# Kernel optimization log

Hardware: AMD Instinct MI355X
Metric: run time of the kernel (lower is better)

Reference implementation:

```python
import jax, jax.numpy as jnp
import numpy as np

S, B, D, H, DH = 2048, 2, 512, 8, 64
SCALE = 1.0 / DH ** 0.5
EPS = 1e-5
LN_EPS = 1e-5


def setup_inputs() -> dict:
    key = jax.random.key(0)
    k1, k2, k3, k4 = jax.random.split(key, 4)
    h = jax.random.normal(k1, (S, B, D), dtype=jnp.float32)
    # causal mask, True = masked out, shape [qlen, klen, 1] (dim==3 branch)
    attn_mask = jnp.triu(jnp.ones((S, S), dtype=bool), k=1)[:, :, None]
    Wq = jax.random.normal(k2, (D, H * DH), dtype=jnp.float32) * 0.02
    Wkv = jax.random.normal(k3, (D, 2 * H * DH), dtype=jnp.float32) * 0.02
    Wo = jax.random.normal(k4, (H * DH, D), dtype=jnp.float32) * 0.02
    gamma = jnp.ones((D,), dtype=jnp.float32)
    beta = jnp.zeros((D,), dtype=jnp.float32)
    return {"h": h, "Wq": Wq, "Wkv": Wkv, "Wo": Wo,
            "gamma": gamma, "beta": beta, "attn_mask": attn_mask}


def _layer_norm(x, gamma, beta):
    mu = jnp.mean(x, axis=-1, keepdims=True)
    var = jnp.mean(jnp.square(x - mu), axis=-1, keepdims=True)
    return (x - mu) * jax.lax.rsqrt(var + LN_EPS) * gamma + beta


def reference(h, Wq, Wkv, Wo, gamma, beta, attn_mask):
    # mems=None, pre_lnorm=False, dropout=dropatt=0 (eval)
    c = h
    head_q = (h @ Wq).reshape(S, B, H, DH)
    kv = (c @ Wkv)
    head_k, head_v = jnp.split(kv, 2, axis=-1)
    head_k = head_k.reshape(S, B, H, DH)
    head_v = head_v.reshape(S, B, H, DH)
    # elu(x) + 1 feature map
    head_q = jax.nn.elu(head_q) + 1.0
    head_k = jax.nn.elu(head_k) + 1.0
    # quadratic score matrix [i, j, b, n]
    attn_score = jnp.einsum('ibnd,jbnd->ijbn', head_q, head_k) * SCALE
    # dim==3 mask: [qlen, klen, 1] -> [qlen, klen, 1, 1], fill with 0
    attn_score = jnp.where(attn_mask[:, :, :, None], 0.0, attn_score)
    # sum-normalize over key axis (dim 1 = j)
    denominator = jnp.sum(attn_score, axis=1, keepdims=True) + EPS
    attn_prob = attn_score / denominator
    attn_vec = jnp.einsum('ijbn,jbnd->ibnd', attn_prob, head_v)
    attn_vec = attn_vec.reshape(S, B, H * DH)
    attn_out = attn_vec @ Wo
    # post-lnorm residual
    return _layer_norm(h + attn_out, gamma, beta)
```

## Files before the change

### kernel.cpp

```cpp
#include <hip/hip_runtime.h>
#include <hip/hip_bf16.h>
#include <math.h>

#define SCALE 0.125f
#define EPS 1e-5f
#define LN_EPS 1e-5f

typedef short short8 __attribute__((ext_vector_type(8)));
typedef float floatx4 __attribute__((ext_vector_type(4)));
typedef unsigned short us;

__device__ __forceinline__ float elu1(float x) { return x > 0.f ? x + 1.f : __expf(x); }
__device__ __forceinline__ us f2bf(float f) {
    __hip_bfloat16 b = __float2bfloat16(f);
    return __builtin_bit_cast(us, b);
}
__device__ __forceinline__ void gload_lds16(const void* g, void* lds) {
    __builtin_amdgcn_global_load_lds(
        (const __attribute__((address_space(1))) unsigned int*)g,
        (__attribute__((address_space(3))) unsigned int*)lds, 16, 0, 0);
}
__device__ __forceinline__ floatx4 mfma_bf16(short8 a, short8 b, floatx4 c) {
    return __builtin_amdgcn_mfma_f32_16x16x32_bf16(a, b, c, 0, 0, 0);
}

__global__ __launch_bounds__(256)
void pack_kernel(const float* __restrict__ h, const float* __restrict__ Wq,
                 const float* __restrict__ Wkv, const float* __restrict__ Wo,
                 us* __restrict__ hB, us* __restrict__ WqkvT, us* __restrict__ WoT,
                 us* __restrict__ VTg) {
    const int bid = blockIdx.x, tid = threadIdx.x;
    if (bid < 2048) {
        int idx = bid * 1024 + tid * 4;
        float4 v = *(const float4*)(h + idx);
        ushort4 o;
        o.x = f2bf(v.x); o.y = f2bf(v.y); o.z = f2bf(v.z); o.w = f2bf(v.w);
        *(ushort4*)(hB + idx) = o;
        return;
    }
    if (bid < 2304) {
        __shared__ us T[64][72];
        const float* src; int ld, n0s, k0; us* dst;
        if (bid < 2240) {
            int t2 = bid - 2048;
            int nt = t2 % 24, kt = t2 / 24;
            int n0 = nt * 64; k0 = kt * 64;
            if (n0 < 512) { src = Wq; ld = 512; n0s = n0; }
            else          { src = Wkv; ld = 1024; n0s = n0 - 512; }
            dst = WqkvT + (size_t)n0 * 512;
        } else {
            int t2 = bid - 2240;
            int nt = t2 & 7, kt = t2 >> 3;
            src = Wo; ld = 512; n0s = nt * 64; k0 = kt * 64;
            dst = WoT + (size_t)(nt * 64) * 512;
        }
        {
            int k = tid >> 2, cs = (tid & 3) * 16;
            const float* p = src + (size_t)(k0 + k) * ld + n0s + cs;
#pragma unroll
            for (int q = 0; q < 4; ++q) {
                float4 v = *(const float4*)(p + q * 4);
                T[k][cs + q * 4 + 0] = f2bf(v.x);
                T[k][cs + q * 4 + 1] = f2bf(v.y);
                T[k][cs + q * 4 + 2] = f2bf(v.z);
                T[k][cs + q * 4 + 3] = f2bf(v.w);
            }
        }
        __syncthreads();
        {
            int n = tid >> 2, ks = (tid & 3) * 16;
            __align__(16) us tmp[16];
#pragma unroll
            for (int j = 0; j < 16; ++j) tmp[j] = T[ks + j][n];
            us* po = dst + (size_t)n * 512 + k0 + ks;
            *(uint4*)(po) = *(uint4*)(tmp);
            *(uint4*)(po + 8) = *(uint4*)(tmp + 8);
        }
        return;
    }
    {
        int e = (bid - 2304) * 1024 + tid * 4;
        int chain = e >> 11, s = e & 2047;
        ushort4 o; o.x = 0x3f80; o.y = 0x3f80; o.z = 0x3f80; o.w = 0x3f80;
        *(ushort4*)(VTg + ((size_t)(chain * 80 + 64)) * 2048 + s) = o;
    }
}

__global__ __launch_bounds__(256)
void qkv_gemm(const us* __restrict__ A, const us* __restrict__ BT,
              us* __restrict__ Qg, us* __restrict__ Kg, us* __restrict__ Vg) {
    __shared__ __align__(16) us As[128 * 32];
    __shared__ __align__(16) us Bs[128 * 32];
    const int tid = threadIdx.x;
    const int w = tid >> 6, l = tid & 63;
    const int m0 = blockIdx.y * 128, n0 = blockIdx.x * 128;
    const int wm = (w >> 1) * 64, wn = (w & 1) * 64;
    floatx4 acc[4][4];
#pragma unroll
    for (int i = 0; i < 4; ++i)
#pragma unroll
        for (int j = 0; j < 4; ++j)
#pragma unroll
            for (int e = 0; e < 4; ++e) acc[i][j][e] = 0.f;

    for (int kt = 0; kt < 512; kt += 32) {
        __syncthreads();
#pragma unroll
        for (int r = 0; r < 2; ++r) {
            int slot = (r * 4 + w) * 64 + l;
            int row = slot >> 2, part = slot & 3;
            int g = part ^ (row & 3);
            gload_lds16(A + (size_t)(m0 + row) * 512 + kt + g * 8, As + (r * 4 + w) * 512);
            gload_lds16(BT + (size_t)(n0 + row) * 512 + kt + g * 8, Bs + (r * 4 + w) * 512);
        }
        __syncthreads();
        short8 a[4], b[4];
#pragma unroll
        for (int mi = 0; mi < 4; ++mi) {
            int row = wm + mi * 16 + (l & 15);
            int p = (l >> 4) ^ (row & 3);
            a[mi] = *(const short8*)(As + row * 32 + p * 8);
        }
#pragma unroll
        for (int ni = 0; ni < 4; ++ni) {
            int row = wn + ni * 16 + (l & 15);
            int p = (l >> 4) ^ (row & 3);
            b[ni] = *(const short8*)(Bs + row * 32 + p * 8);
        }
#pragma unroll
        for (int mi = 0; mi < 4; ++mi)
#pragma unroll
            for (int ni = 0; ni < 4; ++ni)
                acc[mi][ni] = mfma_bf16(a[mi], b[ni], acc[mi][ni]);
    }
    const int region = blockIdx.x >> 2;
    us* outp = region == 0 ? Qg : (region == 1 ? Kg : Vg);
    const int cb = n0 - region * 512;
#pragma unroll
    for (int mi = 0; mi < 4; ++mi)
#pragma unroll
        for (int ni = 0; ni < 4; ++ni)
#pragma unroll
            for (int r = 0; r < 4; ++r) {
                int row = m0 + wm + mi * 16 + (l >> 4) * 4 + r;
                int col = cb + wn + ni * 16 + (l & 15);
                float v = acc[mi][ni][r];
                if (region < 2) v = elu1(v);
                outp[(size_t)row * 512 + col] = f2bf(v);
            }
}

__global__ __launch_bounds__(256)
void chunk_kv_kernel(const us* __restrict__ Kg, const us* __restrict__ Vg,
                     float* __restrict__ KVc, us* __restrict__ VTg) {
    __shared__ __align__(16) us VT_l[80 * 72];
    __shared__ __align__(16) us KT_l[64 * 72];
    const int c = blockIdx.x, chain = blockIdx.y;
    const int b = chain >> 3, hh = chain & 7;
    const int tid = threadIdx.x;
    const int w = tid >> 6, l = tid & 63;
#pragma unroll
    for (int gi = 0; gi < 2; ++gi) {
        int g = w + gi * 4;
        __align__(16) us vv[8];
        __align__(16) us kk[8];
#pragma unroll
        for (int e = 0; e < 8; ++e) {
            size_t off = (size_t)((c * 64 + g * 8 + e) * 2 + b) * 512 + hh * 64 + l;
            vv[e] = Vg[off];
            kk[e] = Kg[off];
        }
        *(uint4*)(VT_l + l * 72 + g * 8) = *(uint4*)vv;
        *(uint4*)(KT_l + l * 72 + g * 8) = *(uint4*)kk;
        *(uint4*)(VTg + ((size_t)(chain * 80 + l)) * 2048 + c * 64 + g * 8) = *(uint4*)vv;
    }
    if (tid < 8) {
        ushort4 o; o.x = 0x3f80; o.y = 0x3f80; o.z = 0x3f80; o.w = 0x3f80;
        *(ushort4*)(VT_l + 64 * 72 + tid * 8) = o;
        *(ushort4*)(VT_l + 64 * 72 + tid * 8 + 4) = o;
    }
    __syncthreads();
    const int l15 = l & 15, l4 = l >> 4;
    short8 af[5][2], bfr[2];
#pragma unroll
    for (int mi = 0; mi < 5; ++mi) {
        int row = mi * 16 + l15;
        af[mi][0] = *(const short8*)(VT_l + row * 72 + l4 * 8);
        af[mi][1] = *(const short8*)(VT_l + row * 72 + 32 + l4 * 8);
    }
    {
        int row = w * 16 + l15;
        bfr[0] = *(const short8*)(KT_l + row * 72 + l4 * 8);
        bfr[1] = *(const short8*)(KT_l + row * 72 + 32 + l4 * 8);
    }
    float* out = KVc + (size_t)(chain * 32 + c) * 4608;
#pragma unroll
    for (int mi = 0; mi < 5; ++mi) {
        floatx4 a = {0.f, 0.f, 0.f, 0.f};
        a = mfma_bf16(af[mi][0], bfr[0], a);
        a = mfma_bf16(af[mi][1], bfr[1], a);
#pragma unroll
        for (int r = 0; r < 4; ++r) {
            int row = mi * 16 + l4 * 4 + r;
            if (row < 65) out[row * 64 + w * 16 + l15] = a[r];
        }
    }
}

__global__ __launch_bounds__(256)
void cumsum_kernel(const float* __restrict__ KVc, us* __restrict__ MTg) {
    const int chain = blockIdx.x, rg = blockIdx.y;
    const int row = rg * 4 + (threadIdx.x >> 6), col = threadIdx.x & 63;
    const float* in = KVc + (size_t)chain * 32 * 4608 + row * 64 + col;
    us* out = MTg + ((size_t)chain * 32 * 80 + row) * 64 + col;
    float acc = 0.f;
#pragma unroll 4
    for (int cc = 0; cc < 32; ++cc) {
        out[(size_t)cc * 5120] = f2bf(acc);
        acc += in[(size_t)cc * 4608];
    }
}

__global__ __launch_bounds__(256)
void attn_kernel(const us* __restrict__ Qg, const us* __restrict__ Kg,
                 const us* __restrict__ VTg, const us* __restrict__ MTg,
                 us* __restrict__ ATT) {
    __shared__ __align__(16) us Qs[64 * 64];
    __shared__ __align__(16) us Ks[64 * 64];
    __shared__ __align__(16) us Vs[80 * 64];
    __shared__ __align__(16) us Ms[80 * 64];
    __shared__ __align__(16) us Sl[64 * 64];
    const int c = blockIdx.x, chain = blockIdx.y;
    const int b = chain >> 3, hh = chain & 7;
    const int tid = threadIdx.x;
    const int w = tid >> 6, l = tid & 63;
    const int l15 = l & 15, l4 = l >> 4;
    const int lrow = l >> 3, lg = l & 7;

#pragma unroll
    for (int r = 0; r < 2; ++r) {
        int slot = r * 4 + w;
        int row = slot * 8 + lrow;
        int g = lg ^ (row & 7);
        size_t grow = (size_t)((c * 64 + row) * 2 + b) * 512 + hh * 64 + g * 8;
        gload_lds16(Qg + grow, Qs + slot * 512);
        gload_lds16(Kg + grow, Ks + slot * 512);
    }
#pragma unroll
    for (int r = 0; r < 3; ++r) {
        int slot = r * 4 + w;
        if (slot < 10) {
            int row = slot * 8 + lrow;
            int g = lg ^ (row & 7);
            gload_lds16(VTg + (size_t)(chain * 80 + row) * 2048 + c * 64 + g * 8,
                        Vs + slot * 512);
            gload_lds16(MTg + ((size_t)(chain * 32 + c) * 80 + row) * 64 + g * 8,
                        Ms + slot * 512);
        }
    }
    __syncthreads();

    short8 qf[2];
    {
        int row = w * 16 + l15, p = l4 ^ (row & 7);
        qf[0] = *(const short8*)(Qs + row * 64 + p * 8);
        qf[1] = *(const short8*)(Qs + row * 64 + (p ^ 4) * 8);
    }
    short8 kf[4][2];
#pragma unroll
    for (int ni = 0; ni < 4; ++ni) {
        int row = ni * 16 + l15, p = l4 ^ (row & 7);
        kf[ni][0] = *(const short8*)(Ks + row * 64 + p * 8);
        kf[ni][1] = *(const short8*)(Ks + row * 64 + (p ^ 4) * 8);
    }
    short8 vf[5][2], mf[5][2];
#pragma unroll
    for (int ni = 0; ni < 5; ++ni) {
        int row = ni * 16 + l15, p = l4 ^ (row & 7);
        vf[ni][0] = *(const short8*)(Vs + row * 64 + p * 8);
        vf[ni][1] = *(const short8*)(Vs + row * 64 + (p ^ 4) * 8);
        mf[ni][0] = *(const short8*)(Ms + row * 64 + p * 8);
        mf[ni][1] = *(const short8*)(Ms + row * 64 + (p ^ 4) * 8);
    }

    const int ibase = w * 16 + l4 * 4;
#pragma unroll
    for (int ni = 0; ni < 4; ++ni) {
        floatx4 s = {0.f, 0.f, 0.f, 0.f};
        s = mfma_bf16(qf[0], kf[ni][0], s);
        s = mfma_bf16(qf[1], kf[ni][1], s);
        int col = ni * 16 + l15;
#pragma unroll
        for (int r = 0; r < 4; ++r) {
            int i = ibase + r;
            float v = (col <= i) ? s[r] : 0.f;
            Sl[i * 64 + (((col >> 3) ^ (i & 7)) * 8) + (col & 7)] = f2bf(v);
        }
    }
    __syncthreads();

    short8 sf[2];
    {
        int ir = w * 16 + l15;
        sf[0] = *(const short8*)(Sl + ir * 64 + ((l4 ^ (ir & 7)) * 8));
        sf[1] = *(const short8*)(Sl + ir * 64 + (((4 + l4) ^ (ir & 7)) * 8));
    }

    floatx4 acc[5];
#pragma unroll
    for (int ni = 0; ni < 5; ++ni) {
        floatx4 a = {0.f, 0.f, 0.f, 0.f};
        a = mfma_bf16(sf[0], vf[ni][0], a);
        a = mfma_bf16(sf[1], vf[ni][1], a);
        a = mfma_bf16(qf[0], mf[ni][0], a);
        a = mfma_bf16(qf[1], mf[ni][1], a);
        acc[ni] = a;
    }

    float fac[4];
#pragma unroll
    for (int r = 0; r < 4; ++r) {
        float den = __shfl(acc[4][r], l & 48, 64);
        fac[r] = SCALE / (SCALE * den + EPS);
    }
#pragma unroll
    for (int ni = 0; ni < 4; ++ni)
#pragma unroll
        for (int r = 0; r < 4; ++r) {
            int i = ibase + r;
            ATT[((size_t)((c * 64 + i) * 2 + b)) * 512 + hh * 64 + ni * 16 + l15] =
                f2bf(acc[ni][r] * fac[r]);
        }
}

__global__ __launch_bounds__(256)
void wo_ln_kernel(const us* __restrict__ ATT, const us* __restrict__ WoT,
                  const float* __restrict__ h, const float* __restrict__ gamma,
                  const float* __restrict__ beta, float* __restrict__ out) {
    __shared__ __align__(16) us As[32 * 32];
    __shared__ __align__(16) us Bs[512 * 32];
    __shared__ float redS[4][32];
    __shared__ float redQ[4][32];
    __shared__ float mml[32], rsl[32];
    const int tid = threadIdx.x;
    const int w = tid >> 6, l = tid & 63;
    const int l15 = l & 15, l4 = l >> 4;
    const int m0 = blockIdx.x * 32, wn = w * 128;
    floatx4 acc[2][8];
#pragma unroll
    for (int i = 0; i < 2; ++i)
#pragma unroll
        for (int j = 0; j < 8; ++j)
#pragma unroll
            for (int e = 0; e < 4; ++e) acc[i][j][e] = 0.f;

    for (int kt = 0; kt < 512; kt += 32) {
        __syncthreads();
#pragma unroll
        for (int r = 0; r < 8; ++r) {
            int slot = r * 4 + w;
            int row = slot * 16 + (l >> 2);
            int g = (l & 3) ^ (row & 3);
            gload_lds16(WoT + (size_t)row * 512 + kt + g * 8, Bs + slot * 512);
        }
        if (w < 2) {
            int row = w * 16 + (l >> 2);
            int g = (l & 3) ^ (row & 3);
            gload_lds16(ATT + (size_t)(m0 + row) * 512 + kt + g * 8, As + w * 512);
        }
        __syncthreads();
        short8 af[2], bf[8];
#pragma unroll
        for (int mi = 0; mi < 2; ++mi) {
            int row = mi * 16 + l15, p = l4 ^ (row & 3);
            af[mi] = *(const short8*)(As + row * 32 + p * 8);
        }
#pragma unroll
        for (int ni = 0; ni < 8; ++ni) {
            int row = wn + ni * 16 + l15, p = l4 ^ (row & 3);
            bf[ni] = *(const short8*)(Bs + row * 32 + p * 8);
        }
#pragma unroll
        for (int mi = 0; mi < 2; ++mi)
#pragma unroll
            for (int ni = 0; ni < 8; ++ni)
                acc[mi][ni] = mfma_bf16(af[mi], bf[ni], acc[mi][ni]);
    }

#pragma unroll
    for (int mi = 0; mi < 2; ++mi)
#pragma unroll
        for (int r = 0; r < 4; ++r) {
            int row = mi * 16 + l4 * 4 + r;
            const float* hrow = h + (size_t)(m0 + row) * 512 + wn + l15;
            float s = 0.f, q = 0.f;
#pragma unroll
            for (int ni = 0; ni < 8; ++ni) {
                float x = acc[mi][ni][r] + hrow[ni * 16];
                acc[mi][ni][r] = x;
                s += x;
                q = fmaf(x, x, q);
            }
#pragma unroll
            for (int off = 1; off <= 8; off <<= 1) {
                s += __shfl_xor(s, off, 64);
                q += __shfl_xor(q, off, 64);
            }
            if (l15 == 0) { redS[w][row] = s; redQ[w][row] = q; }
        }
    __syncthreads();
    if (tid < 32) {
        float s = redS[0][tid] + redS[1][tid] + redS[2][tid] + redS[3][tid];
        float q = redQ[0][tid] + redQ[1][tid] + redQ[2][tid] + redQ[3][tid];
        float mean = s * (1.f / 512);
        float var = q * (1.f / 512) - mean * mean;
        mml[tid] = mean;
        rsl[tid] = rsqrtf(var + LN_EPS);
    }
    __syncthreads();
#pragma unroll
    for (int mi = 0; mi < 2; ++mi)
#pragma unroll
        for (int r = 0; r < 4; ++r) {
            int row = mi * 16 + l4 * 4 + r;
            float mean = mml[row], rstd = rsl[row];
#pragma unroll
            for (int ni = 0; ni < 8; ++ni) {
                int col = wn + ni * 16 + l15;
                out[(size_t)(m0 + row) * 512 + col] =
                    (acc[mi][ni][r] - mean) * rstd * gamma[col] + beta[col];
            }
        }
}

extern "C" void kernel_launch(void* const* d_in, const int* in_sizes, int n_in,
                              void* d_out, int out_size, void* d_ws, size_t ws_size,
                              hipStream_t stream) {
    const float* h = (const float*)d_in[0];
    const float* Wq = (const float*)d_in[1];
    const float* Wkv = (const float*)d_in[2];
    const float* Wo = (const float*)d_in[3];
    const float* gamma = (const float*)d_in[4];
    const float* beta = (const float*)d_in[5];

    char* ws = (char*)d_ws;
    us* Qg      = (us*)(ws + 0);
    us* Kg      = (us*)(ws + 4194304);
    us* Vg      = (us*)(ws + 8388608);
    us* VTg     = (us*)(ws + 12582912);
    us* ATT     = (us*)(ws + 17825792);
    us* WoT     = (us*)(ws + 22020096);
    us* MTg     = (us*)(ws + 22544384);
    us* hB      = (us*)(ws + 27787264);
    us* WqkvT   = (us*)(ws + 31981568);
    float* KVc  = (float*)(ws + 33554432);

    dim3 blk(256);
    pack_kernel<<<2336, blk, 0, stream>>>(h, Wq, Wkv, Wo, hB, WqkvT, WoT, VTg);
    qkv_gemm<<<dim3(12, 32), blk, 0, stream>>>(hB, WqkvT, Qg, Kg, Vg);
    chunk_kv_kernel<<<dim3(32, 16), blk, 0, stream>>>(Kg, Vg, KVc, VTg);
    cumsum_kernel<<<dim3(16, 17), blk, 0, stream>>>(KVc, MTg);
    attn_kernel<<<dim3(32, 16), blk, 0, stream>>>(Qg, Kg, VTg, MTg, ATT);
    wo_ln_kernel<<<128, blk, 0, stream>>>(ATT, WoT, h, gamma, beta, (float*)d_out);
}
```

Baseline: 139.1 us.

## Double-buffer LDS in QKV and Wo GEMMs, halve Wo row tile for more blocks

Both GEMM kernels now keep two LDS buffers and issue the global-to-LDS loads for the next K slice before computing on the current one, so load latency overlaps with MFMA work. The Wo+LayerNorm kernel also drops from 32 to 16 rows per block, doubling the grid from 128 to 256 blocks to fill more CUs. The cost is more LDS per block (about 66KB in the Wo kernel, which can limit occupancy) and twice as many reads of the full Wo weight tile across blocks.

```diff
diff --git a/kernel.cpp b/kernel.cpp
--- a/kernel.cpp
+++ b/kernel.cpp
@@ -89,8 +89,8 @@
 __global__ __launch_bounds__(256)
 void qkv_gemm(const us* __restrict__ A, const us* __restrict__ BT,
               us* __restrict__ Qg, us* __restrict__ Kg, us* __restrict__ Vg) {
-    __shared__ __align__(16) us As[128 * 32];
-    __shared__ __align__(16) us Bs[128 * 32];
+    __shared__ __align__(16) us As[2][128 * 32];
+    __shared__ __align__(16) us Bs[2][128 * 32];
     const int tid = threadIdx.x;
     const int w = tid >> 6, l = tid & 63;
     const int m0 = blockIdx.y * 128, n0 = blockIdx.x * 128;
@@ -103,35 +103,41 @@
 #pragma unroll
             for (int e = 0; e < 4; ++e) acc[i][j][e] = 0.f;
 
-    for (int kt = 0; kt < 512; kt += 32) {
-        __syncthreads();
+    auto STAGE = [&](int buf, int kt) {
 #pragma unroll
         for (int r = 0; r < 2; ++r) {
             int slot = (r * 4 + w) * 64 + l;
             int row = slot >> 2, part = slot & 3;
             int g = part ^ (row & 3);
-            gload_lds16(A + (size_t)(m0 + row) * 512 + kt + g * 8, As + (r * 4 + w) * 512);
-            gload_lds16(BT + (size_t)(n0 + row) * 512 + kt + g * 8, Bs + (r * 4 + w) * 512);
-        }
-        __syncthreads();
+            gload_lds16(A + (size_t)(m0 + row) * 512 + kt + g * 8, &As[buf][(r * 4 + w) * 512]);
+            gload_lds16(BT + (size_t)(n0 + row) * 512 + kt + g * 8, &Bs[buf][(r * 4 + w) * 512]);
+        }
+    };
+
+    STAGE(0, 0);
+    __syncthreads();
+    for (int t = 0; t < 16; ++t) {
+        int cur = t & 1;
+        if (t < 15) STAGE(cur ^ 1, (t + 1) * 32);
         short8 a[4], b[4];
 #pragma unroll
         for (int mi = 0; mi < 4; ++mi) {
             int row = wm + mi * 16 + (l & 15);
             int p = (l >> 4) ^ (row & 3);
-            a[mi] = *(const short8*)(As + row * 32 + p * 8);
+            a[mi] = *(const short8*)(&As[cur][row * 32 + p * 8]);
         }
 #pragma unroll
         for (int ni = 0; ni < 4; ++ni) {
             int row = wn + ni * 16 + (l & 15);
             int p = (l >> 4) ^ (row & 3);
-            b[ni] = *(const short8*)(Bs + row * 32 + p * 8);
+            b[ni] = *(const short8*)(&Bs[cur][row * 32 + p * 8]);
         }
 #pragma unroll
         for (int mi = 0; mi < 4; ++mi)
 #pragma unroll
             for (int ni = 0; ni < 4; ++ni)
                 acc[mi][ni] = mfma_bf16(a[mi], b[ni], acc[mi][ni]);
+        __syncthreads();
     }
     const int region = blockIdx.x >> 2;
     us* outp = region == 0 ? Qg : (region == 1 ? Kg : Vg);
@@ -337,79 +343,78 @@
 void wo_ln_kernel(const us* __restrict__ ATT, const us* __restrict__ WoT,
                   const float* __restrict__ h, const float* __restrict__ gamma,
                   const float* __restrict__ beta, float* __restrict__ out) {
-    __shared__ __align__(16) us As[32 * 32];
-    __shared__ __align__(16) us Bs[512 * 32];
-    __shared__ float redS[4][32];
-    __shared__ float redQ[4][32];
-    __shared__ float mml[32], rsl[32];
+    __shared__ __align__(16) us As[2][16 * 32];
+    __shared__ __align__(16) us Bs[2][512 * 32];
+    __shared__ float redS[4][16];
+    __shared__ float redQ[4][16];
+    __shared__ float mml[16], rsl[16];
     const int tid = threadIdx.x;
     const int w = tid >> 6, l = tid & 63;
     const int l15 = l & 15, l4 = l >> 4;
-    const int m0 = blockIdx.x * 32, wn = w * 128;
-    floatx4 acc[2][8];
-#pragma unroll
-    for (int i = 0; i < 2; ++i)
-#pragma unroll
-        for (int j = 0; j < 8; ++j)
-#pragma unroll
-            for (int e = 0; e < 4; ++e) acc[i][j][e] = 0.f;
-
-    for (int kt = 0; kt < 512; kt += 32) {
-        __syncthreads();
+    const int m0 = blockIdx.x * 16, wn = w * 128;
+    floatx4 acc[8];
+#pragma unroll
+    for (int j = 0; j < 8; ++j)
+#pragma unroll
+        for (int e = 0; e < 4; ++e) acc[j][e] = 0.f;
+
+    auto STAGE = [&](int buf, int kt) {
 #pragma unroll
         for (int r = 0; r < 8; ++r) {
             int slot = r * 4 + w;
             int row = slot * 16 + (l >> 2);
             int g = (l & 3) ^ (row & 3);
-            gload_lds16(WoT + (size_t)row * 512 + kt + g * 8, Bs + slot * 512);
-        }
-        if (w < 2) {
-            int row = w * 16 + (l >> 2);
+            gload_lds16(WoT + (size_t)row * 512 + kt + g * 8, &Bs[buf][slot * 512]);
+        }
+        if (w == 0) {
+            int row = l >> 2;
             int g = (l & 3) ^ (row & 3);
-            gload_lds16(ATT + (size_t)(m0 + row) * 512 + kt + g * 8, As + w * 512);
-        }
-        __syncthreads();
-        short8 af[2], bf[8];
-#pragma unroll
-        for (int mi = 0; mi < 2; ++mi) {
-            int row = mi * 16 + l15, p = l4 ^ (row & 3);
-            af[mi] = *(const short8*)(As + row * 32 + p * 8);
+            gload_lds16(ATT + (size_t)(m0 + row) * 512 + kt + g * 8, &As[buf][0]);
+        }
+    };
+
+    STAGE(0, 0);
+    __syncthreads();
+    for (int t = 0; t < 16; ++t) {
+        int cur = t & 1;
+        if (t < 15) STAGE(cur ^ 1, (t + 1) * 32);
+        short8 af, bf[8];
+        {
+            int row = l15, p = l4 ^ (row & 3);
+            af = *(const short8*)(&As[cur][row * 32 + p * 8]);
         }
 #pragma unroll
         for (int ni = 0; ni < 8; ++ni) {
             int row = wn + ni * 16 + l15, p = l4 ^ (row & 3);
-            bf[ni] = *(const short8*)(Bs + row * 32 + p * 8);
-        }
-#pragma unroll
-        for (int mi = 0; mi < 2; ++mi)
-#pragma unroll
-            for (int ni = 0; ni < 8; ++ni)
-                acc[mi][ni] = mfma_bf16(af[mi], bf[ni], acc[mi][ni]);
-    }
-
-#pragma unroll
-    for (int mi = 0; mi < 2; ++mi)
-#pragma unroll
-        for (int r = 0; r < 4; ++r) {
-            int row = mi * 16 + l4 * 4 + r;
-            const float* hrow = h + (size_t)(m0 + row) * 512 + wn + l15;
-            float s = 0.f, q = 0.f;
-#pragma unroll
-            for (int ni = 0; ni < 8; ++ni) {
-                float x = acc[mi][ni][r] + hrow[ni * 16];
-                acc[mi][ni][r] = x;
-                s += x;
-                q = fmaf(x, x, q);
-            }
-#pragma unroll
-            for (int off = 1; off <= 8; off <<= 1) {
-                s += __shfl_xor(s, off, 64);
-                q += __shfl_xor(q, off, 64);
-            }
-            if (l15 == 0) { redS[w][row] = s; redQ[w][row] = q; }
-        }
-    __syncthreads();
-    if (tid < 32) {
+            bf[ni] = *(const short8*)(&Bs[cur][row * 32 + p * 8]);
+        }
+#pragma unroll
+        for (int ni = 0; ni < 8; ++ni)
+            acc[ni] = mfma_bf16(af, bf[ni], acc[ni]);
+        __syncthreads();
+    }
+
+#pragma unroll
+    for (int r = 0; r < 4; ++r) {
+        int row = l4 * 4 + r;
+        const float* hrow = h + (size_t)(m0 + row) * 512 + wn + l15;
+        float s = 0.f, q = 0.f;
+#pragma unroll
+        for (int ni = 0; ni < 8; ++ni) {
+            float x = acc[ni][r] + hrow[ni * 16];
+            acc[ni][r] = x;
+            s += x;
+            q = fmaf(x, x, q);
+        }
+#pragma unroll
+        for (int off = 1; off <= 8; off <<= 1) {
+            s += __shfl_xor(s, off, 64);
+            q += __shfl_xor(q, off, 64);
+        }
+        if (l15 == 0) { redS[w][row] = s; redQ[w][row] = q; }
+    }
+    __syncthreads();
+    if (tid < 16) {
         float s = redS[0][tid] + redS[1][tid] + redS[2][tid] + redS[3][tid];
         float q = redQ[0][tid] + redQ[1][tid] + redQ[2][tid] + redQ[3][tid];
         float mean = s * (1.f / 512);
@@ -419,18 +424,16 @@
     }
     __syncthreads();
 #pragma unroll
-    for (int mi = 0; mi < 2; ++mi)
-#pragma unroll
-        for (int r = 0; r < 4; ++r) {
-            int row = mi * 16 + l4 * 4 + r;
-            float mean = mml[row], rstd = rsl[row];
-#pragma unroll
-            for (int ni = 0; ni < 8; ++ni) {
-                int col = wn + ni * 16 + l15;
-                out[(size_t)(m0 + row) * 512 + col] =
-                    (acc[mi][ni][r] - mean) * rstd * gamma[col] + beta[col];
-            }
-        }
+    for (int r = 0; r < 4; ++r) {
+        int row = l4 * 4 + r;
+        float mean = mml[row], rstd = rsl[row];
+#pragma unroll
+        for (int ni = 0; ni < 8; ++ni) {
+            int col = wn + ni * 16 + l15;
+            out[(size_t)(m0 + row) * 512 + col] =
+                (acc[ni][r] - mean) * rstd * gamma[col] + beta[col];
+        }
+    }
 }
 
 extern "C" void kernel_launch(void* const* d_in, const int* in_sizes, int n_in,
@@ -461,5 +464,5 @@
     chunk_kv_kernel<<<dim3(32, 16), blk, 0, stream>>>(Kg, Vg, KVc, VTg);
     cumsum_kernel<<<dim3(16, 17), blk, 0, stream>>>(KVc, MTg);
     attn_kernel<<<dim3(32, 16), blk, 0, stream>>>(Qg, Kg, VTg, MTg, ATT);
-    wo_ln_kernel<<<128, blk, 0, stream>>>(ATT, WoT, h, gamma, beta, (float*)d_out);
-}
+    wo_ln_kernel<<<256, blk, 0, stream>>>(ATT, WoT, h, gamma, beta, (float*)d_out);
+}
```

Measured after the change: 134.7 us. -3.1%, faster.
